# Performance work log

Measured on AMD Instinct MI355X. Metric: run time of the kernel, lower is better.

The kernel has to match this reference:

```python
import jax, jax.numpy as jnp
import numpy as np

N_UP, N_DN = 64, 64
L = 10.0
BATCH = 8192


def _create_centers(N_up, N_dn, L):
    n = 1
    while n ** 3 < max(N_up, N_dn):
        n += 1
    a = L / n
    coords = np.linspace(0.0, L - a, n)
    grid = np.stack(np.meshgrid(coords, coords, coords, indexing='ij'), axis=-1).reshape(-1, 3)
    centers_up = grid[:N_up]
    centers_dn = (grid + a / 2.0)[:N_dn]
    return jnp.asarray(centers_up, jnp.float32), jnp.asarray(centers_dn, jnp.float32)


def _slater_logdet(rs_spin, centers, alpha):
    # rs_spin: [B, N, 3], centers: [M, 3] -> Phi: [B, N, M]
    dr = rs_spin[:, :, None, :] - centers[None, None, :, :]
    dr_p = (L / jnp.pi) * jnp.sin(jnp.pi * dr / L)  # smooth periodic displacement
    r2 = jnp.sum(dr_p * dr_p, axis=-1)
    Phi = jnp.exp(-alpha * r2)
    _, logdet = jnp.linalg.slogdet(Phi)
    return logdet  # [B]


def setup_inputs() -> dict:
    key = jax.random.key(0)
    k1, _ = jax.random.split(key)
    rs = jax.random.uniform(k1, (BATCH, N_UP + N_DN, 3), dtype=jnp.float32) * L
    log_alpha = jnp.asarray(np.log(np.sqrt(100.0) / L ** 2), dtype=jnp.float32)
    return {"rs": rs, "log_alpha": log_alpha}


def reference(rs, log_alpha):
    centers_up, centers_dn = _create_centers(N_UP, N_DN, L)
    alpha = jnp.exp(log_alpha)
    alpha = jnp.clip(alpha, 0.5 / L ** 2, 200.0 / L ** 2)
    log_up = _slater_logdet(rs[:, :N_UP], centers_up, alpha)
    log_dn = _slater_logdet(rs[:, N_UP:N_UP + N_DN], centers_dn, alpha)
    return log_up + log_dn  # [B]
```

## Files before the change

kernel.cpp:

```cpp
#include <hip/hip_runtime.h>

__device__ __forceinline__ int rdlane_i(int v, int l) {
    return __builtin_amdgcn_readlane(v, l);
}
__device__ __forceinline__ float rdlane_f(float v, int l) {
    return __int_as_float(__builtin_amdgcn_readlane(__float_as_int(v), l));
}

template <int CTRL>
__device__ __forceinline__ int dpp_imax_step(int x) {
    int t = __builtin_amdgcn_update_dpp(0, x, CTRL, 0xF, 0xF, true);
    return (t > x) ? t : x;
}

__device__ __forceinline__ int wave_imax_to_lane63(int x) {
    x = dpp_imax_step<0xB1>(x);
    x = dpp_imax_step<0x4E>(x);
    x = dpp_imax_step<0x141>(x);
    x = dpp_imax_step<0x140>(x);
    x = dpp_imax_step<0x142>(x);
    x = dpp_imax_step<0x143>(x);
    return x;
}

__global__ __launch_bounds__(128, 3) void slater_logdet_kernel(
        const float* __restrict__ rs, const float* __restrict__ log_alpha_p,
        float* __restrict__ out) {
    const int b    = blockIdx.x;
    const int tid  = threadIdx.x;
    const int wave = tid >> 6;
    const int lane = tid & 63;

    const float Lbox = 10.0f;
    const float PI_F = 3.14159265358979323846f;

    float alpha = __expf(log_alpha_p[0]);
    alpha = fminf(fmaxf(alpha, 0.5f / (Lbox * Lbox)), 200.0f / (Lbox * Lbox));

    const float* rp = rs + (size_t)b * 384 + (size_t)(wave * 64 + lane) * 3;
    float x = rp[0], y = rp[1], z = rp[2];

    float sx, cx, sy, cy, sz, cz;
    __sincosf(x * (PI_F / Lbox), &sx, &cx);
    __sincosf(y * (PI_F / Lbox), &sy, &cy);
    __sincosf(z * (PI_F / Lbox), &sz, &cz);

    const float off = wave ? 0.5f : 0.0f;
    const float LPI = Lbox / PI_F;
    float ex[4], ey[4], ez[4];
#pragma unroll
    for (int m = 0; m < 4; ++m) {
        float sp, cp;
        __sincosf((PI_F * 0.25f) * ((float)m + off), &sp, &cp);
        float dx = LPI * (sx * cp - cx * sp);
        float dy = LPI * (sy * cp - cy * sp);
        float dz = LPI * (sz * cp - cz * sp);
        ex[m] = __expf(-alpha * dx * dx);
        ey[m] = __expf(-alpha * dy * dy);
        ez[m] = __expf(-alpha * dz * dz);
    }
    float exy[16];
#pragma unroll
    for (int q = 0; q < 16; ++q) exy[q] = ex[q >> 2] * ey[q & 3];
    float A[64];
#pragma unroll
    for (int j = 0; j < 64; ++j) A[j] = exy[j >> 2] * ez[j & 3];

    float flag   = 0.0f;
    float logdet = 0.0f;
#pragma unroll
    for (int k = 0; k < 64; ++k) {
        float key = fabsf(A[k]) + flag;
        int   ki  = (__float_as_int(key) & ~63) | lane;
        int   g   = rdlane_i(wave_imax_to_lane63(ki), 63);
        int   p   = g & 63;

        float pv  = rdlane_f(A[k], p);
        float inv = __builtin_amdgcn_rcpf(pv);
        inv = inv * (2.0f - pv * inv);
        logdet += __logf(fabsf(pv));

        flag = (lane == p) ? -__builtin_huge_valf() : flag;

        float m = A[k] * inv;
#pragma unroll
        for (int j = k + 1; j < 64; ++j) {
            float s = rdlane_f(A[j], p);
            A[j] = __builtin_fmaf(-m, s, A[j]);
        }
    }

    __shared__ float partial[2];
    if (lane == 0) partial[wave] = logdet;
    __syncthreads();
    if (tid == 0) out[b] = partial[0] + partial[1];
}

extern "C" void kernel_launch(void* const* d_in, const int* in_sizes, int n_in,
                              void* d_out, int out_size, void* d_ws, size_t ws_size,
                              hipStream_t stream) {
    const float* rs = (const float*)d_in[0];
    const float* la = (const float*)d_in[1];
    float* out      = (float*)d_out;
    slater_logdet_kernel<<<out_size, 128, 0, stream>>>(rs, la, out);
}
```

Baseline: 287.3 us.

## Split each 64x64 LU across two waves with interleaved columns

Each spin determinant is now factorised by two waves, each owning alternating columns (32 registers instead of 64). The wave owning column k picks the pivot and multipliers, publishes them through shared memory, and both waves update their own columns after a block-wide barrier. This halves the per-wave update work and register pressure, at the cost of 64 __syncthreads per block and LDS traffic that serialise the pivot step.

```diff
diff --git a/kernel.cpp b/kernel.cpp
--- a/kernel.cpp
+++ b/kernel.cpp
@@ -23,12 +23,14 @@
     return x;
 }
 
-__global__ __launch_bounds__(128, 3) void slater_logdet_kernel(
+__global__ __launch_bounds__(256, 4) void slater_logdet_kernel(
         const float* __restrict__ rs, const float* __restrict__ log_alpha_p,
         float* __restrict__ out) {
     const int b    = blockIdx.x;
     const int tid  = threadIdx.x;
-    const int wave = tid >> 6;
+    const int wv   = tid >> 6;
+    const int spin = wv >> 1;
+    const int w    = wv & 1;
     const int lane = tid & 63;
 
     const float Lbox = 10.0f;
@@ -37,7 +39,7 @@
     float alpha = __expf(log_alpha_p[0]);
     alpha = fminf(fmaxf(alpha, 0.5f / (Lbox * Lbox)), 200.0f / (Lbox * Lbox));
 
-    const float* rp = rs + (size_t)b * 384 + (size_t)(wave * 64 + lane) * 3;
+    const float* rp = rs + (size_t)b * 384 + (size_t)(spin * 64 + lane) * 3;
     float x = rp[0], y = rp[1], z = rp[2];
 
     float sx, cx, sy, cy, sz, cz;
@@ -45,7 +47,7 @@
     __sincosf(y * (PI_F / Lbox), &sy, &cy);
     __sincosf(z * (PI_F / Lbox), &sz, &cz);
 
-    const float off = wave ? 0.5f : 0.0f;
+    const float off = spin ? 0.5f : 0.0f;
     const float LPI = Lbox / PI_F;
     float ex[4], ey[4], ez[4];
 #pragma unroll
@@ -59,41 +61,65 @@
         ey[m] = __expf(-alpha * dy * dy);
         ez[m] = __expf(-alpha * dz * dz);
     }
-    float exy[16];
+
+    float A[32];
+    if (w == 0) {
 #pragma unroll
-    for (int q = 0; q < 16; ++q) exy[q] = ex[q >> 2] * ey[q & 3];
-    float A[64];
+        for (int t = 0; t < 32; ++t) {
+            const int j = 2 * t;
+            A[t] = ex[j >> 4] * ey[(j >> 2) & 3] * ez[j & 3];
+        }
+    } else {
 #pragma unroll
-    for (int j = 0; j < 64; ++j) A[j] = exy[j >> 2] * ez[j & 3];
+        for (int t = 0; t < 32; ++t) {
+            const int j = 2 * t + 1;
+            A[t] = ex[j >> 4] * ey[(j >> 2) & 3] * ez[j & 3];
+        }
+    }
+
+    __shared__ float mbuf[2][2][64];
+    __shared__ int   pbuf[2][2];
+    __shared__ float partial[4];
 
     float flag   = 0.0f;
     float logdet = 0.0f;
 #pragma unroll
     for (int k = 0; k < 64; ++k) {
-        float key = fabsf(A[k]) + flag;
-        int   ki  = (__float_as_int(key) & ~63) | lane;
-        int   g   = rdlane_i(wave_imax_to_lane63(ki), 63);
-        int   p   = g & 63;
+        const int par = k & 1;
+        int   ps = 0;
+        float m  = 0.0f;
+        if (w == par) {
+            const int tk = k >> 1;
+            float key = fabsf(A[tk]) + flag;
+            int   ki  = (__float_as_int(key) & ~63) | lane;
+            int   g   = rdlane_i(wave_imax_to_lane63(ki), 63);
+            ps = g & 63;
+            float pv  = rdlane_f(A[tk], ps);
+            float inv = __builtin_amdgcn_rcpf(pv);
+            inv = inv * (2.0f - pv * inv);
+            logdet += __logf(fabsf(pv));
+            m = A[tk] * inv;
+            mbuf[spin][par][lane] = m;
+            if (lane == 0) pbuf[spin][par] = ps;
+        }
+        __syncthreads();
+        if (w != par) {
+            m  = mbuf[spin][par][lane];
+            ps = __builtin_amdgcn_readfirstlane(pbuf[spin][par]);
+        }
 
-        float pv  = rdlane_f(A[k], p);
-        float inv = __builtin_amdgcn_rcpf(pv);
-        inv = inv * (2.0f - pv * inv);
-        logdet += __logf(fabsf(pv));
+        flag = (lane == ps) ? -__builtin_huge_valf() : flag;
 
-        flag = (lane == p) ? -__builtin_huge_valf() : flag;
-
-        float m = A[k] * inv;
 #pragma unroll
-        for (int j = k + 1; j < 64; ++j) {
-            float s = rdlane_f(A[j], p);
-            A[j] = __builtin_fmaf(-m, s, A[j]);
+        for (int t = (k >> 1); t < 32; ++t) {
+            float s = rdlane_f(A[t], ps);
+            A[t] = __builtin_fmaf(-m, s, A[t]);
         }
     }
 
-    __shared__ float partial[2];
-    if (lane == 0) partial[wave] = logdet;
+    if (lane == 0) partial[wv] = logdet;
     __syncthreads();
-    if (tid == 0) out[b] = partial[0] + partial[1];
+    if (tid == 0) out[b] = partial[0] + partial[1] + partial[2] + partial[3];
 }
 
 extern "C" void kernel_launch(void* const* d_in, const int* in_sizes, int n_in,
@@ -102,5 +128,5 @@
     const float* rs = (const float*)d_in[0];
     const float* la = (const float*)d_in[1];
     float* out      = (float*)d_out;
-    slater_logdet_kernel<<<out_size, 128, 0, stream>>>(rs, la, out);
+    slater_logdet_kernel<<<out_size, 256, 0, stream>>>(rs, la, out);
 }
```

Measured after the change: 307.3 us. 7.0% more time.
